# Performance work log

Measured on AMD Instinct MI355X. Metric: run time of the kernel, lower is better.

Reference implementation:

```python
import jax, jax.numpy as jnp
import numpy as np

HEADS = 8

def setup_inputs() -> dict:
    key = jax.random.key(0)
    ks = jax.random.split(key, 6)
    b, c, w, h = 4, 512, 48, 48
    qc, vc = 512, 512
    s = 1.0 / np.sqrt(c)  # orthogonal-init-like scale for 1x1 conv weights
    return {
        "x": jax.random.normal(ks[0], (b, c, w, h), dtype=jnp.float32),
        "Wq": jax.random.normal(ks[1], (qc, c), dtype=jnp.float32) * s,
        "Wk": jax.random.normal(ks[2], (qc, c), dtype=jnp.float32) * s,
        "Wv": jax.random.normal(ks[3], (vc, c), dtype=jnp.float32) * s,
        "Wsc": jax.random.normal(ks[4], (vc, c), dtype=jnp.float32) * s,
        "gamma": jax.random.normal(ks[5], (1, vc, 1, 1), dtype=jnp.float32),
    }


def reference(x, Wq, Wk, Wv, Wsc, gamma):
    b, c, w, h = x.shape
    n = w * h
    dq = Wq.shape[0] // HEADS
    dv = Wv.shape[0] // HEADS
    # 1x1 convs are channel matmuls
    q = jnp.einsum('bchw,oc->bohw', x, Wq).reshape(b, HEADS, dq, n)
    k = jnp.einsum('bchw,oc->bohw', x, Wk).reshape(b, HEADS, dq, n)
    v = jnp.einsum('bchw,oc->bohw', x, Wv).reshape(b, HEADS, dv, n)
    # attention scores over spatial tokens (no scaling in original)
    attn = jax.nn.softmax(jnp.einsum('bhdn,bhdm->bhnm', q, k), axis=-1)
    out = jnp.einsum('bhnm,bhdm->bnhd', attn, v)  # (b, n, heads, dv)
    out = out.reshape(b, w, h, HEADS * dv).transpose(0, 3, 1, 2)  # head-major channels
    sc = jnp.einsum('bchw,oc->bohw', x, Wsc)
    return gamma * out + sc
```

## Files before the change

kernel.cpp:

```cpp
#include <hip/hip_runtime.h>

#define HEADS 8
static constexpr int BSZ = 4;
static constexpr int CCH = 512;
static constexpr int NSP = 2304;
static constexpr int DH  = 64;

typedef _Float16 f16x8 __attribute__((ext_vector_type(8)));
typedef _Float16 f16x2 __attribute__((ext_vector_type(2)));
typedef float f32x4 __attribute__((ext_vector_type(4)));
typedef float f32x16 __attribute__((ext_vector_type(16)));
typedef int i32x4 __attribute__((ext_vector_type(4)));
typedef unsigned short u16;
typedef unsigned int u32;

__device__ __forceinline__ u16 f2h(float f) {
  _Float16 h = (_Float16)f;
  return __builtin_bit_cast(u16, h);
}

__device__ __forceinline__ void gl_lds16(const void* g, void* l) {
  __builtin_amdgcn_global_load_lds(
      (const __attribute__((address_space(1))) u32*)g,
      (__attribute__((address_space(3))) u32*)l, 16, 0, 0);
}

__global__ void k_cvt_w(const float* __restrict__ w0, const float* __restrict__ w1,
                        const float* __restrict__ w2, const float* __restrict__ w3,
                        u16* __restrict__ dst) {
  int wsel = blockIdx.y;
  const float* src = wsel == 0 ? w0 : wsel == 1 ? w1 : wsel == 2 ? w2 : w3;
  int i = (blockIdx.x * 256 + threadIdx.x) * 4;
  float4 v = *(const float4*)(src + i);
  ushort4 o;
  o.x = f2h(v.x); o.y = f2h(v.y); o.z = f2h(v.z); o.w = f2h(v.w);
  *(ushort4*)(dst + (size_t)wsel * CCH * CCH + i) = o;
}

__global__ void k_cvt_x(const float* __restrict__ x, u16* __restrict__ xT) {
  __shared__ u16 t[64][66];
  int b = blockIdx.z, c0 = blockIdx.y * 64, n0 = blockIdx.x * 64;
  int col = threadIdx.x & 63, rb = threadIdx.x >> 6;
#pragma unroll
  for (int rr = 0; rr < 16; rr++) {
    int r = rr * 4 + rb;
    t[r][col] = f2h(x[((size_t)b * CCH + c0 + r) * NSP + n0 + col]);
  }
  __syncthreads();
#pragma unroll
  for (int rr = 0; rr < 16; rr++) {
    int r = rr * 4 + rb;
    xT[((size_t)b * NSP + n0 + r) * CCH + c0 + col] = t[col][r];
  }
}

__global__ __launch_bounds__(256) void k_proj(const u16* __restrict__ Wall,
    const u16* __restrict__ xT, u16* __restrict__ Qo, u16* __restrict__ Ko,
    u16* __restrict__ Vo, float* __restrict__ SCo) {
  __shared__ u16 smem[17408];
  u16* At = smem;
  u16* Bt = smem + 8192;
  int z = blockIdx.z, b = z >> 2, wsel = z & 3;
  int o0 = blockIdx.y * 128, n0 = blockIdx.x * 128;
  int tid = threadIdx.x, lane = tid & 63, wv = tid >> 6;
  int wr = wv >> 1, wc = wv & 1;
  const u16* Asrc = Wall + (size_t)wsel * CCH * CCH + (size_t)o0 * CCH;
  const u16* Bsrc = xT + ((size_t)b * NSP + n0) * CCH;
  f32x4 acc[4][4] = {};
  for (int kc = 0; kc < CCH; kc += 64) {
    __syncthreads();
#pragma unroll
    for (int i = 0; i < 4; i++) {
      int ch = (wv * 4 + i) * 64 + lane;
      int row = ch >> 3, cc = ch & 7;
      gl_lds16(Asrc + (size_t)row * CCH + kc + ((cc ^ (row & 7)) << 3), At + (wv * 4 + i) * 512);
      gl_lds16(Bsrc + (size_t)row * CCH + kc + ((cc ^ (row & 7)) << 3), Bt + (wv * 4 + i) * 512);
    }
    __syncthreads();
#pragma unroll
    for (int ks = 0; ks < 2; ks++) {
      f16x8 af[4], bfr[4];
#pragma unroll
      for (int f = 0; f < 4; f++) {
        int orow = wr * 64 + f * 16 + (lane & 15);
        int nrow = wc * 64 + f * 16 + (lane & 15);
        int k8 = (lane >> 4) + ks * 4;
        af[f]  = *(const f16x8*)(At + orow * 64 + ((k8 ^ (orow & 7)) << 3));
        bfr[f] = *(const f16x8*)(Bt + nrow * 64 + ((k8 ^ (nrow & 7)) << 3));
      }
#pragma unroll
      for (int i = 0; i < 4; i++)
#pragma unroll
        for (int j = 0; j < 4; j++)
          acc[i][j] = __builtin_amdgcn_mfma_f32_16x16x32_f16(af[i], bfr[j], acc[i][j], 0, 0, 0);
    }
  }
  if (wsel >= 2) {
#pragma unroll
    for (int i = 0; i < 4; i++)
#pragma unroll
      for (int j = 0; j < 4; j++)
#pragma unroll
        for (int r = 0; r < 4; r++) {
          int o = o0 + wr * 64 + i * 16 + ((lane >> 4) << 2) + r;
          int n = n0 + wc * 64 + j * 16 + (lane & 15);
          size_t idx = ((size_t)b * CCH + o) * NSP + n;
          if (wsel == 3) SCo[idx] = acc[i][j][r];
          else           Vo[idx]  = f2h(acc[i][j][r]);
        }
  } else {
    __syncthreads();
    u16* stash = smem;
#pragma unroll
    for (int i = 0; i < 4; i++)
#pragma unroll
      for (int j = 0; j < 4; j++)
#pragma unroll
        for (int r = 0; r < 4; r++) {
          int ol = wr * 64 + i * 16 + ((lane >> 4) << 2) + r;
          int nl = wc * 64 + j * 16 + (lane & 15);
          stash[nl * 136 + ol] = f2h(acc[i][j][r]);
        }
    __syncthreads();
    u16* dst = wsel ? Ko : Qo;
    int hl = tid >> 7, nn = tid & 127;
    int h = (o0 >> 6) + hl;
    size_t base = ((size_t)(b * HEADS + h) * NSP + n0 + nn) * DH;
#pragma unroll
    for (int c2 = 0; c2 < 8; c2++)
      *(int4*)(dst + base + c2 * 8) = *(const int4*)(stash + nn * 136 + hl * 64 + c2 * 8);
  }
}

__device__ __forceinline__ void stage_kv(const u16* Ksrc, const u16* Vsrc,
                                         u16* Kb, u16* Vb, int bsel, int m0, int tid) {
#pragma unroll
  for (int i = 0; i < 4; i++) {
    int ch = i * 128 + tid;
    int row = ch >> 3, cc = ch & 7;
    gl_lds16(Ksrc + (size_t)(m0 + row) * DH + ((cc ^ (row & 7)) << 3),
             Kb + bsel * 4096 + ch * 8);
    gl_lds16(Vsrc + (size_t)row * NSP + m0 + ((cc ^ (row & 7)) << 3),
             Vb + bsel * 4096 + ch * 8);
  }
}

__global__ __launch_bounds__(128) void k_attn(const u16* __restrict__ Qw,
    const u16* __restrict__ Kw, const u16* __restrict__ Vw,
    const float* __restrict__ gamma, float* __restrict__ out) {
  __shared__ u16 smem[16384];
  u16* Kb = smem;
  u16* Vb = smem + 8192;
  int qt = blockIdx.x, bh = blockIdx.y;
  int b = bh >> 3, h = bh & 7;
  int tid = threadIdx.x, lane = tid & 63, wv = tid >> 6;
  int l31 = lane & 31, hi = lane >> 5;
  int q0w = qt * 64 + wv * 32;
  const u16* Ksrc = Kw + (size_t)bh * NSP * DH;
  const u16* Vsrc = Vw + ((size_t)b * CCH + h * DH) * NSP;

  f16x8 qf[4];
  const u16* Qbase = Qw + ((size_t)bh * NSP + q0w + l31) * DH + hi * 8;
#pragma unroll
  for (int kd = 0; kd < 4; kd++)
    qf[kd] = *(const f16x8*)(Qbase + kd * 16);

  float mrun = -1e30f, lrun = 0.f;
  f32x16 acc0 = {}, acc1 = {};

  stage_kv(Ksrc, Vsrc, Kb, Vb, 0, 0, tid);
  __syncthreads();

  for (int mt = 0; mt < NSP / 64; mt++) {
    int cur = mt & 1;
    if (mt + 1 < NSP / 64) stage_kv(Ksrc, Vsrc, Kb, Vb, cur ^ 1, (mt + 1) * 64, tid);

    f32x16 s0 = {}, s1 = {};
#pragma unroll
    for (int kd = 0; kd < 4; kd++) {
      int cc = 2 * kd + hi;
      int r0 = l31, r1 = 32 + l31;
      f16x8 k0 = *(const f16x8*)(Kb + cur * 4096 + r0 * 64 + ((cc ^ (r0 & 7)) << 3));
      f16x8 k1 = *(const f16x8*)(Kb + cur * 4096 + r1 * 64 + ((cc ^ (r1 & 7)) << 3));
      s0 = __builtin_amdgcn_mfma_f32_32x32x16_f16(k0, qf[kd], s0, 0, 0, 0);
      s1 = __builtin_amdgcn_mfma_f32_32x32x16_f16(k1, qf[kd], s1, 0, 0, 0);
    }

    float tm = fmaxf(s0[0], s1[0]);
#pragma unroll
    for (int r = 1; r < 16; r++) tm = fmaxf(tm, fmaxf(s0[r], s1[r]));
    tm = fmaxf(tm, __shfl_xor(tm, 32));
    if (__any(tm > mrun + 8.0f)) {
      float mnew = fmaxf(mrun, tm);
      float scl = __expf(mrun - mnew);
      mrun = mnew;
      lrun *= scl;
#pragma unroll
      for (int r = 0; r < 16; r++) {
        float sq = __shfl(scl, (r & 3) + 8 * (r >> 2) + 4 * hi);
        acc0[r] *= sq;
        acc1[r] *= sq;
      }
    }
    float ts = 0.f;
    u32 P2[2][4][2];
#pragma unroll
    for (int s2 = 0; s2 < 4; s2++)
#pragma unroll
      for (int c = 0; c < 2; c++) {
        float a0 = __expf(s0[4 * s2 + 2 * c] - mrun);
        float b0 = __expf(s0[4 * s2 + 2 * c + 1] - mrun);
        float a1 = __expf(s1[4 * s2 + 2 * c] - mrun);
        float b1 = __expf(s1[4 * s2 + 2 * c + 1] - mrun);
        ts += (a0 + b0) + (a1 + b1);
        P2[0][s2][c] = __builtin_bit_cast(u32, __builtin_amdgcn_cvt_pkrtz(a0, b0));
        P2[1][s2][c] = __builtin_bit_cast(u32, __builtin_amdgcn_cvt_pkrtz(a1, b1));
      }
    ts += __shfl_xor(ts, 32);
    lrun += ts;

#pragma unroll
    for (int s = 0; s < 4; s++) {
      int blk = s >> 1, par = s & 1;
      int T[4];
#pragma unroll
      for (int c = 0; c < 2; c++) {
        int x = (int)P2[blk][2 * par][c];
        int y = (int)P2[blk][2 * par + 1][c];
        int xs = __shfl_xor(x, 32);
        int ys = __shfl_xor(y, 32);
        T[c]     = hi ? ys : x;
        T[c + 2] = hi ? y  : xs;
      }
      f16x8 pa = __builtin_bit_cast(f16x8, (i32x4){T[0], T[1], T[2], T[3]});
      int ccv = 2 * s + hi;
      {
        int row = l31;
        f16x8 vb = *(const f16x8*)(Vb + cur * 4096 + row * 64 + ((ccv ^ (row & 7)) << 3));
        acc0 = __builtin_amdgcn_mfma_f32_32x32x16_f16(pa, vb, acc0, 0, 0, 0);
      }
      {
        int row = 32 + l31;
        f16x8 vb = *(const f16x8*)(Vb + cur * 4096 + row * 64 + ((ccv ^ (row & 7)) << 3));
        acc1 = __builtin_amdgcn_mfma_f32_32x32x16_f16(pa, vb, acc1, 0, 0, 0);
      }
    }
    __syncthreads();
  }

  float inv = 1.0f / lrun;
  float invq[16];
#pragma unroll
  for (int r = 0; r < 16; r++)
    invq[r] = __shfl(inv, (r & 3) + 8 * (r >> 2) + 4 * hi);
  size_t outbase = ((size_t)b * CCH + h * DH) * NSP;
#pragma unroll
  for (int dblk = 0; dblk < 2; dblk++) {
    int d = dblk * 32 + l31;
    float g = gamma[h * DH + d];
    float* orow = out + outbase + (size_t)d * NSP + q0w;
#pragma unroll
    for (int s2 = 0; s2 < 4; s2++) {
      int n = 8 * s2 + 4 * hi;
      f32x4 o;
#pragma unroll
      for (int t = 0; t < 4; t++) {
        int r = 4 * s2 + t;
        float a = dblk ? acc1[r] : acc0[r];
        o[t] = a * invq[r] * g;
      }
      f32x4 sc = *(const f32x4*)(orow + n);
      *(f32x4*)(orow + n) = o + sc;
    }
  }
}

extern "C" void kernel_launch(void* const* d_in, const int* in_sizes, int n_in,
                              void* d_out, int out_size, void* d_ws, size_t ws_size,
                              hipStream_t stream) {
  const float* x     = (const float*)d_in[0];
  const float* Wq    = (const float*)d_in[1];
  const float* Wk    = (const float*)d_in[2];
  const float* Wv    = (const float*)d_in[3];
  const float* Wsc   = (const float*)d_in[4];
  const float* gamma = (const float*)d_in[5];
  float* out = (float*)d_out;

  u16* xT   = (u16*)d_ws;
  u16* Wall = xT + (size_t)BSZ * NSP * CCH;
  u16* Qw   = Wall + (size_t)4 * CCH * CCH;
  u16* Kw   = Qw + (size_t)BSZ * CCH * NSP;
  u16* Vw   = Kw + (size_t)BSZ * CCH * NSP;

  hipLaunchKernelGGL(k_cvt_w, dim3(CCH * CCH / 1024, 4), dim3(256), 0, stream,
                     Wq, Wk, Wv, Wsc, Wall);
  hipLaunchKernelGGL(k_cvt_x, dim3(NSP / 64, CCH / 64, BSZ), dim3(256), 0, stream, x, xT);
  hipLaunchKernelGGL(k_proj, dim3(NSP / 128, CCH / 128, BSZ * 4), dim3(256), 0, stream,
                     Wall, xT, Qw, Kw, Vw, out);
  hipLaunchKernelGGL(k_attn, dim3(NSP / 64, BSZ * HEADS), dim3(128), 0, stream,
                     Qw, Kw, Vw, gamma, out);
}
```

Measured before the change: 172.4 us.

## Split attention KV range across two wave groups and fold log2e into Q

```diff
diff --git a/kernel.cpp b/kernel.cpp
--- a/kernel.cpp
+++ b/kernel.cpp
@@ -7,7 +7,6 @@
 static constexpr int DH  = 64;
 
 typedef _Float16 f16x8 __attribute__((ext_vector_type(8)));
-typedef _Float16 f16x2 __attribute__((ext_vector_type(2)));
 typedef float f32x4 __attribute__((ext_vector_type(4)));
 typedef float f32x16 __attribute__((ext_vector_type(16)));
 typedef int i32x4 __attribute__((ext_vector_type(4)));
@@ -111,6 +110,7 @@
   } else {
     __syncthreads();
     u16* stash = smem;
+    float qs = (wsel == 0) ? 1.4426950408889634f : 1.0f;
 #pragma unroll
     for (int i = 0; i < 4; i++)
 #pragma unroll
@@ -119,7 +119,7 @@
         for (int r = 0; r < 4; r++) {
           int ol = wr * 64 + i * 16 + ((lane >> 4) << 2) + r;
           int nl = wc * 64 + j * 16 + (lane & 15);
-          stash[nl * 136 + ol] = f2h(acc[i][j][r]);
+          stash[nl * 136 + ol] = f2h(acc[i][j][r] * qs);
         }
     __syncthreads();
     u16* dst = wsel ? Ko : Qo;
@@ -132,32 +132,32 @@
   }
 }
 
-__device__ __forceinline__ void stage_kv(const u16* Ksrc, const u16* Vsrc,
-                                         u16* Kb, u16* Vb, int bsel, int m0, int tid) {
-#pragma unroll
-  for (int i = 0; i < 4; i++) {
-    int ch = i * 128 + tid;
+__device__ __forceinline__ void stage_kv256(const u16* Ksrc, const u16* Vsrc,
+                                            u16* Kb, u16* Vb, int m0, int gid) {
+#pragma unroll
+  for (int i = 0; i < 2; i++) {
+    int ch = i * 256 + gid;
     int row = ch >> 3, cc = ch & 7;
-    gl_lds16(Ksrc + (size_t)(m0 + row) * DH + ((cc ^ (row & 7)) << 3),
-             Kb + bsel * 4096 + ch * 8);
-    gl_lds16(Vsrc + (size_t)row * NSP + m0 + ((cc ^ (row & 7)) << 3),
-             Vb + bsel * 4096 + ch * 8);
-  }
-}
-
-__global__ __launch_bounds__(128) void k_attn(const u16* __restrict__ Qw,
+    gl_lds16(Ksrc + (size_t)(m0 + row) * DH + ((cc ^ (row & 7)) << 3), Kb + ch * 8);
+    gl_lds16(Vsrc + (size_t)row * NSP + m0 + ((cc ^ (row & 7)) << 3), Vb + ch * 8);
+  }
+}
+
+__global__ __launch_bounds__(512, 4) void k_attn(const u16* __restrict__ Qw,
     const u16* __restrict__ Kw, const u16* __restrict__ Vw,
     const float* __restrict__ gamma, float* __restrict__ out) {
-  __shared__ u16 smem[16384];
-  u16* Kb = smem;
-  u16* Vb = smem + 8192;
+  __shared__ u16 smem[32768];
   int qt = blockIdx.x, bh = blockIdx.y;
   int b = bh >> 3, h = bh & 7;
   int tid = threadIdx.x, lane = tid & 63, wv = tid >> 6;
   int l31 = lane & 31, hi = lane >> 5;
-  int q0w = qt * 64 + wv * 32;
+  int qh = wv & 3, tp = wv >> 2;
+  int gid = tid & 255;
+  int q0w = qt * 128 + qh * 32;
   const u16* Ksrc = Kw + (size_t)bh * NSP * DH;
   const u16* Vsrc = Vw + ((size_t)b * CCH + h * DH) * NSP;
+  u16* Kb = smem + tp * 16384;
+  u16* Vb = Kb + 8192;
 
   f16x8 qf[4];
   const u16* Qbase = Qw + ((size_t)bh * NSP + q0w + l31) * DH + hi * 8;
@@ -168,31 +168,39 @@
   float mrun = -1e30f, lrun = 0.f;
   f32x16 acc0 = {}, acc1 = {};
 
-  stage_kv(Ksrc, Vsrc, Kb, Vb, 0, 0, tid);
+  stage_kv256(Ksrc, Vsrc, Kb, Vb, tp * 64, gid);
   __syncthreads();
 
-  for (int mt = 0; mt < NSP / 64; mt++) {
-    int cur = mt & 1;
-    if (mt + 1 < NSP / 64) stage_kv(Ksrc, Vsrc, Kb, Vb, cur ^ 1, (mt + 1) * 64, tid);
+  const int NT = NSP / 128;
+  for (int it = 0; it < NT; it++) {
+    int cur = it & 1;
+    if (it + 1 < NT)
+      stage_kv256(Ksrc, Vsrc, Kb + (cur ^ 1) * 4096, Vb + (cur ^ 1) * 4096,
+                  (tp + 2 * (it + 1)) * 64, gid);
+    const u16* Kc = Kb + cur * 4096;
+    const u16* Vc = Vb + cur * 4096;
 
     f32x16 s0 = {}, s1 = {};
 #pragma unroll
     for (int kd = 0; kd < 4; kd++) {
       int cc = 2 * kd + hi;
       int r0 = l31, r1 = 32 + l31;
-      f16x8 k0 = *(const f16x8*)(Kb + cur * 4096 + r0 * 64 + ((cc ^ (r0 & 7)) << 3));
-      f16x8 k1 = *(const f16x8*)(Kb + cur * 4096 + r1 * 64 + ((cc ^ (r1 & 7)) << 3));
+      f16x8 k0 = *(const f16x8*)(Kc + r0 * 64 + ((cc ^ (r0 & 7)) << 3));
+      f16x8 k1 = *(const f16x8*)(Kc + r1 * 64 + ((cc ^ (r1 & 7)) << 3));
       s0 = __builtin_amdgcn_mfma_f32_32x32x16_f16(k0, qf[kd], s0, 0, 0, 0);
       s1 = __builtin_amdgcn_mfma_f32_32x32x16_f16(k1, qf[kd], s1, 0, 0, 0);
     }
 
-    float tm = fmaxf(s0[0], s1[0]);
-#pragma unroll
-    for (int r = 1; r < 16; r++) tm = fmaxf(tm, fmaxf(s0[r], s1[r]));
+    float a8[8];
+#pragma unroll
+    for (int i = 0; i < 8; i++)
+      a8[i] = fmaxf(fmaxf(s0[2 * i], s0[2 * i + 1]), fmaxf(s1[2 * i], s1[2 * i + 1]));
+    float tm = fmaxf(fmaxf(fmaxf(a8[0], a8[1]), fmaxf(a8[2], a8[3])),
+                     fmaxf(fmaxf(a8[4], a8[5]), fmaxf(a8[6], a8[7])));
     tm = fmaxf(tm, __shfl_xor(tm, 32));
-    if (__any(tm > mrun + 8.0f)) {
+    if (__any(tm > mrun + 11.5f)) {
       float mnew = fmaxf(mrun, tm);
-      float scl = __expf(mrun - mnew);
+      float scl = exp2f(mrun - mnew);
       mrun = mnew;
       lrun *= scl;
 #pragma unroll
@@ -202,20 +210,21 @@
         acc1[r] *= sq;
       }
     }
-    float ts = 0.f;
+    float tsp[4] = {0.f, 0.f, 0.f, 0.f};
     u32 P2[2][4][2];
 #pragma unroll
     for (int s2 = 0; s2 < 4; s2++)
 #pragma unroll
       for (int c = 0; c < 2; c++) {
-        float a0 = __expf(s0[4 * s2 + 2 * c] - mrun);
-        float b0 = __expf(s0[4 * s2 + 2 * c + 1] - mrun);
-        float a1 = __expf(s1[4 * s2 + 2 * c] - mrun);
-        float b1 = __expf(s1[4 * s2 + 2 * c + 1] - mrun);
-        ts += (a0 + b0) + (a1 + b1);
+        float a0 = exp2f(s0[4 * s2 + 2 * c] - mrun);
+        float b0 = exp2f(s0[4 * s2 + 2 * c + 1] - mrun);
+        float a1 = exp2f(s1[4 * s2 + 2 * c] - mrun);
+        float b1 = exp2f(s1[4 * s2 + 2 * c + 1] - mrun);
+        tsp[s2] += (a0 + b0) + (a1 + b1);
         P2[0][s2][c] = __builtin_bit_cast(u32, __builtin_amdgcn_cvt_pkrtz(a0, b0));
         P2[1][s2][c] = __builtin_bit_cast(u32, __builtin_amdgcn_cvt_pkrtz(a1, b1));
       }
+    float ts = (tsp[0] + tsp[1]) + (tsp[2] + tsp[3]);
     ts += __shfl_xor(ts, 32);
     lrun += ts;
 
@@ -236,41 +245,65 @@
       int ccv = 2 * s + hi;
       {
         int row = l31;
-        f16x8 vb = *(const f16x8*)(Vb + cur * 4096 + row * 64 + ((ccv ^ (row & 7)) << 3));
+        f16x8 vb = *(const f16x8*)(Vc + row * 64 + ((ccv ^ (row & 7)) << 3));
         acc0 = __builtin_amdgcn_mfma_f32_32x32x16_f16(pa, vb, acc0, 0, 0, 0);
       }
       {
         int row = 32 + l31;
-        f16x8 vb = *(const f16x8*)(Vb + cur * 4096 + row * 64 + ((ccv ^ (row & 7)) << 3));
+        f16x8 vb = *(const f16x8*)(Vc + row * 64 + ((ccv ^ (row & 7)) << 3));
         acc1 = __builtin_amdgcn_mfma_f32_32x32x16_f16(pa, vb, acc1, 0, 0, 0);
       }
     }
     __syncthreads();
   }
 
-  float inv = 1.0f / lrun;
-  float invq[16];
-#pragma unroll
-  for (int r = 0; r < 16; r++)
-    invq[r] = __shfl(inv, (r & 3) + 8 * (r >> 2) + 4 * hi);
-  size_t outbase = ((size_t)b * CCH + h * DH) * NSP;
-#pragma unroll
-  for (int dblk = 0; dblk < 2; dblk++) {
-    int d = dblk * 32 + l31;
-    float g = gamma[h * DH + d];
-    float* orow = out + outbase + (size_t)d * NSP + q0w;
-#pragma unroll
-    for (int s2 = 0; s2 < 4; s2++) {
-      int n = 8 * s2 + 4 * hi;
-      f32x4 o;
-#pragma unroll
-      for (int t = 0; t < 4; t++) {
-        int r = 4 * s2 + t;
-        float a = dblk ? acc1[r] : acc0[r];
-        o[t] = a * invq[r] * g;
-      }
-      f32x4 sc = *(const f32x4*)(orow + n);
-      *(f32x4*)(orow + n) = o + sc;
+  float* sf = (float*)smem;
+  if (tp) {
+#pragma unroll
+    for (int r = 0; r < 16; r++) {
+      sf[qh * 2048 + r * 64 + lane] = acc0[r];
+      sf[qh * 2048 + (16 + r) * 64 + lane] = acc1[r];
+    }
+    if (lane < 32) {
+      sf[8192 + qh * 64 + l31] = mrun;
+      sf[8192 + qh * 64 + 32 + l31] = lrun;
+    }
+  }
+  __syncthreads();
+  if (!tp) {
+    float mb = sf[8192 + qh * 64 + l31];
+    float lb = sf[8192 + qh * 64 + 32 + l31];
+    float M = fmaxf(mrun, mb);
+    float fa = exp2f(mrun - M), fb = exp2f(mb - M);
+    float linv = 1.0f / (lrun * fa + lb * fb);
+    fa *= linv; fb *= linv;
+    float faq[16], fbq[16];
+#pragma unroll
+    for (int r = 0; r < 16; r++) {
+      int qloc = (r & 3) + 8 * (r >> 2) + 4 * hi;
+      faq[r] = __shfl(fa, qloc);
+      fbq[r] = __shfl(fb, qloc);
+    }
+    size_t outbase = ((size_t)b * CCH + h * DH) * NSP;
+#pragma unroll
+    for (int dblk = 0; dblk < 2; dblk++) {
+      int d = dblk * 32 + l31;
+      float g = gamma[h * DH + d];
+      float* orow = out + outbase + (size_t)d * NSP + q0w;
+#pragma unroll
+      for (int s2 = 0; s2 < 4; s2++) {
+        int n = 8 * s2 + 4 * hi;
+        f32x4 o;
+#pragma unroll
+        for (int t = 0; t < 4; t++) {
+          int r = 4 * s2 + t;
+          float oa = dblk ? acc1[r] : acc0[r];
+          float ob = sf[qh * 2048 + (dblk * 16 + r) * 64 + lane];
+          o[t] = (oa * faq[r] + ob * fbq[r]) * g;
+        }
+        f32x4 sc = *(const f32x4*)(orow + n);
+        *(f32x4*)(orow + n) = o + sc;
+      }
     }
   }
 }
@@ -297,6 +330,6 @@
   hipLaunchKernelGGL(k_cvt_x, dim3(NSP / 64, CCH / 64, BSZ), dim3(256), 0, stream, x, xT);
   hipLaunchKernelGGL(k_proj, dim3(NSP / 128, CCH / 128, BSZ * 4), dim3(256), 0, stream,
                      Wall, xT, Qw, Kw, Vw, out);
-  hipLaunchKernelGGL(k_attn, dim3(NSP / 64, BSZ * HEADS), dim3(128), 0, stream,
+  hipLaunchKernelGGL(k_attn, dim3(NSP / 128, BSZ * HEADS), dim3(512), 0, stream,
                      Qw, Kw, Vw, gamma, out);
 }
```

New measurement: 176.3 us. +2.3%, slower.

## Restructure attention loop with 32-key tiles, exp2 softmax, permlane swap, priorities

Applied to the files above, without the earlier changes.

```diff
diff --git a/kernel.cpp b/kernel.cpp
--- a/kernel.cpp
+++ b/kernel.cpp
@@ -7,7 +7,6 @@
 static constexpr int DH  = 64;
 
 typedef _Float16 f16x8 __attribute__((ext_vector_type(8)));
-typedef _Float16 f16x2 __attribute__((ext_vector_type(2)));
 typedef float f32x4 __attribute__((ext_vector_type(4)));
 typedef float f32x16 __attribute__((ext_vector_type(16)));
 typedef int i32x4 __attribute__((ext_vector_type(4)));
@@ -17,6 +16,10 @@
 __device__ __forceinline__ u16 f2h(float f) {
   _Float16 h = (_Float16)f;
   return __builtin_bit_cast(u16, h);
+}
+
+__device__ __forceinline__ float fexp2(float x) {
+  return __builtin_amdgcn_exp2f(x);
 }
 
 __device__ __forceinline__ void gl_lds16(const void* g, void* l) {
@@ -111,6 +114,7 @@
   } else {
     __syncthreads();
     u16* stash = smem;
+    float qs = (wsel == 0) ? 1.4426950408889634f : 1.0f;
 #pragma unroll
     for (int i = 0; i < 4; i++)
 #pragma unroll
@@ -119,7 +123,7 @@
         for (int r = 0; r < 4; r++) {
           int ol = wr * 64 + i * 16 + ((lane >> 4) << 2) + r;
           int nl = wc * 64 + j * 16 + (lane & 15);
-          stash[nl * 136 + ol] = f2h(acc[i][j][r]);
+          stash[nl * 136 + ol] = f2h(acc[i][j][r] * qs);
         }
     __syncthreads();
     u16* dst = wsel ? Ko : Qo;
@@ -132,25 +136,10 @@
   }
 }
 
-__device__ __forceinline__ void stage_kv(const u16* Ksrc, const u16* Vsrc,
-                                         u16* Kb, u16* Vb, int bsel, int m0, int tid) {
-#pragma unroll
-  for (int i = 0; i < 4; i++) {
-    int ch = i * 128 + tid;
-    int row = ch >> 3, cc = ch & 7;
-    gl_lds16(Ksrc + (size_t)(m0 + row) * DH + ((cc ^ (row & 7)) << 3),
-             Kb + bsel * 4096 + ch * 8);
-    gl_lds16(Vsrc + (size_t)row * NSP + m0 + ((cc ^ (row & 7)) << 3),
-             Vb + bsel * 4096 + ch * 8);
-  }
-}
-
 __global__ __launch_bounds__(128) void k_attn(const u16* __restrict__ Qw,
     const u16* __restrict__ Kw, const u16* __restrict__ Vw,
     const float* __restrict__ gamma, float* __restrict__ out) {
-  __shared__ u16 smem[16384];
-  u16* Kb = smem;
-  u16* Vb = smem + 8192;
+  __shared__ u16 smem[8192];
   int qt = blockIdx.x, bh = blockIdx.y;
   int b = bh >> 3, h = bh & 7;
   int tid = threadIdx.x, lane = tid & 63, wv = tid >> 6;
@@ -158,6 +147,35 @@
   int q0w = qt * 64 + wv * 32;
   const u16* Ksrc = Kw + (size_t)bh * NSP * DH;
   const u16* Vsrc = Vw + ((size_t)b * CCH + h * DH) * NSP;
+  u16* Kb0 = smem;
+  u16* Kb1 = smem + 4096;
+
+  int ch0 = tid, ch1 = 128 + tid;
+  int mk0 = ch0 >> 3, pk0 = ch0 & 7, mk1 = ch1 >> 3, pk1 = ch1 & 7;
+  const u16* kc0 = Ksrc + mk0 * DH + ((pk0 ^ (mk0 & 7)) << 3);
+  const u16* kc1 = Ksrc + mk1 * DH + ((pk1 ^ (mk1 & 7)) << 3);
+  int dv0 = ch0 >> 2, pv0 = ch0 & 3, dv1 = ch1 >> 2, pv1 = ch1 & 3;
+  const u16* vc0 = Vsrc + dv0 * NSP + ((pv0 ^ ((dv0 >> 1) & 3)) << 3);
+  const u16* vc1 = Vsrc + dv1 * NSP + ((pv1 ^ ((dv1 >> 1) & 3)) << 3);
+
+#define STAGE(KB)                                  \
+  do {                                             \
+    gl_lds16(kc0, (KB) + ch0 * 8);                 \
+    gl_lds16(kc1, (KB) + ch1 * 8);                 \
+    gl_lds16(vc0, (KB) + 2048 + ch0 * 8);          \
+    gl_lds16(vc1, (KB) + 2048 + ch1 * 8);          \
+    kc0 += 32 * DH; kc1 += 32 * DH;                \
+    vc0 += 32; vc1 += 32;                          \
+  } while (0)
+
+  int kswz = l31 & 7, vswz = (l31 >> 1) & 3;
+  int kro = l31 * 64;
+  int ko[4], vo[2];
+#pragma unroll
+  for (int kd = 0; kd < 4; kd++) ko[kd] = ((2 * kd + hi) ^ kswz) << 3;
+#pragma unroll
+  for (int s = 0; s < 2; s++) vo[s] = ((2 * s + hi) ^ vswz) << 3;
+  int vr0 = l31 * 32, vr1 = (32 + l31) * 32;
 
   f16x8 qf[4];
   const u16* Qbase = Qw + ((size_t)bh * NSP + q0w + l31) * DH + hi * 8;
@@ -168,83 +186,79 @@
   float mrun = -1e30f, lrun = 0.f;
   f32x16 acc0 = {}, acc1 = {};
 
-  stage_kv(Ksrc, Vsrc, Kb, Vb, 0, 0, tid);
+#define COMPUTE(KB)                                                          \
+  do {                                                                       \
+    const u16* Kc = (KB);                                                    \
+    const u16* Vc = (KB) + 2048;                                             \
+    f32x16 s0 = {};                                                          \
+    __builtin_amdgcn_s_setprio(1);                                           \
+    _Pragma("unroll")                                                        \
+    for (int kd = 0; kd < 4; kd++) {                                         \
+      f16x8 k0 = *(const f16x8*)(Kc + kro + ko[kd]);                         \
+      s0 = __builtin_amdgcn_mfma_f32_32x32x16_f16(k0, qf[kd], s0, 0, 0, 0);  \
+    }                                                                        \
+    __builtin_amdgcn_s_setprio(0);                                           \
+    float m0a = fmaxf(fmaxf(s0[0], s0[1]), s0[2]);                           \
+    float m0b = fmaxf(fmaxf(s0[3], s0[4]), s0[5]);                           \
+    float m0c = fmaxf(fmaxf(s0[6], s0[7]), s0[8]);                           \
+    float m0d = fmaxf(fmaxf(s0[9], s0[10]), s0[11]);                         \
+    float m0e = fmaxf(fmaxf(s0[12], s0[13]), s0[14]);                        \
+    float tm = fmaxf(fmaxf(fmaxf(m0a, m0b), fmaxf(m0c, m0d)),                \
+                     fmaxf(m0e, s0[15]));                                    \
+    tm = fmaxf(tm, __shfl_xor(tm, 32));                                      \
+    if (__any(tm > mrun + 11.5f)) {                                          \
+      float mnew = fmaxf(mrun, tm);                                          \
+      float scl = fexp2(mrun - mnew);                                        \
+      mrun = mnew;                                                           \
+      lrun *= scl;                                                           \
+      _Pragma("unroll")                                                      \
+      for (int r = 0; r < 16; r++) {                                         \
+        float sq = __shfl(scl, (r & 3) + 8 * (r >> 2) + 4 * hi);             \
+        acc0[r] *= sq;                                                       \
+        acc1[r] *= sq;                                                       \
+      }                                                                      \
+    }                                                                        \
+    float ts = 0.f;                                                          \
+    u32 P2[4][2];                                                            \
+    _Pragma("unroll")                                                        \
+    for (int s2 = 0; s2 < 4; s2++)                                           \
+      _Pragma("unroll")                                                      \
+      for (int c = 0; c < 2; c++) {                                          \
+        float a = fexp2(s0[4 * s2 + 2 * c] - mrun);                          \
+        float bb = fexp2(s0[4 * s2 + 2 * c + 1] - mrun);                     \
+        ts += a + bb;                                                        \
+        P2[s2][c] = __builtin_bit_cast(u32, __builtin_amdgcn_cvt_pkrtz(a, bb)); \
+      }                                                                      \
+    ts += __shfl_xor(ts, 32);                                                \
+    lrun += ts;                                                              \
+    _Pragma("unroll")                                                        \
+    for (int s = 0; s < 2; s++) {                                            \
+      int x0 = (int)P2[2 * s][0], y0 = (int)P2[2 * s + 1][0];                \
+      int x1 = (int)P2[2 * s][1], y1 = (int)P2[2 * s + 1][1];                \
+      asm("v_permlane32_swap_b32 %0, %1" : "+v"(x0), "+v"(y0));              \
+      asm("v_permlane32_swap_b32 %0, %1" : "+v"(x1), "+v"(y1));              \
+      f16x8 pa = __builtin_bit_cast(f16x8, (i32x4){x0, x1, y0, y1});         \
+      __builtin_amdgcn_s_setprio(1);                                         \
+      {                                                                      \
+        f16x8 vb = *(const f16x8*)(Vc + vr0 + vo[s]);                        \
+        acc0 = __builtin_amdgcn_mfma_f32_32x32x16_f16(pa, vb, acc0, 0, 0, 0);\
+      }                                                                      \
+      {                                                                      \
+        f16x8 vb = *(const f16x8*)(Vc + vr1 + vo[s]);                        \
+        acc1 = __builtin_amdgcn_mfma_f32_32x32x16_f16(pa, vb, acc1, 0, 0, 0);\
+      }                                                                      \
+      __builtin_amdgcn_s_setprio(0);                                         \
+    }                                                                        \
+  } while (0)
+
+  STAGE(Kb0);
   __syncthreads();
-
-  for (int mt = 0; mt < NSP / 64; mt++) {
-    int cur = mt & 1;
-    if (mt + 1 < NSP / 64) stage_kv(Ksrc, Vsrc, Kb, Vb, cur ^ 1, (mt + 1) * 64, tid);
-
-    f32x16 s0 = {}, s1 = {};
-#pragma unroll
-    for (int kd = 0; kd < 4; kd++) {
-      int cc = 2 * kd + hi;
-      int r0 = l31, r1 = 32 + l31;
-      f16x8 k0 = *(const f16x8*)(Kb + cur * 4096 + r0 * 64 + ((cc ^ (r0 & 7)) << 3));
-      f16x8 k1 = *(const f16x8*)(Kb + cur * 4096 + r1 * 64 + ((cc ^ (r1 & 7)) << 3));
-      s0 = __builtin_amdgcn_mfma_f32_32x32x16_f16(k0, qf[kd], s0, 0, 0, 0);
-      s1 = __builtin_amdgcn_mfma_f32_32x32x16_f16(k1, qf[kd], s1, 0, 0, 0);
-    }
-
-    float tm = fmaxf(s0[0], s1[0]);
-#pragma unroll
-    for (int r = 1; r < 16; r++) tm = fmaxf(tm, fmaxf(s0[r], s1[r]));
-    tm = fmaxf(tm, __shfl_xor(tm, 32));
-    if (__any(tm > mrun + 8.0f)) {
-      float mnew = fmaxf(mrun, tm);
-      float scl = __expf(mrun - mnew);
-      mrun = mnew;
-      lrun *= scl;
-#pragma unroll
-      for (int r = 0; r < 16; r++) {
-        float sq = __shfl(scl, (r & 3) + 8 * (r >> 2) + 4 * hi);
-        acc0[r] *= sq;
-        acc1[r] *= sq;
-      }
-    }
-    float ts = 0.f;
-    u32 P2[2][4][2];
-#pragma unroll
-    for (int s2 = 0; s2 < 4; s2++)
-#pragma unroll
-      for (int c = 0; c < 2; c++) {
-        float a0 = __expf(s0[4 * s2 + 2 * c] - mrun);
-        float b0 = __expf(s0[4 * s2 + 2 * c + 1] - mrun);
-        float a1 = __expf(s1[4 * s2 + 2 * c] - mrun);
-        float b1 = __expf(s1[4 * s2 + 2 * c + 1] - mrun);
-        ts += (a0 + b0) + (a1 + b1);
-        P2[0][s2][c] = __builtin_bit_cast(u32, __builtin_amdgcn_cvt_pkrtz(a0, b0));
-        P2[1][s2][c] = __builtin_bit_cast(u32, __builtin_amdgcn_cvt_pkrtz(a1, b1));
-      }
-    ts += __shfl_xor(ts, 32);
-    lrun += ts;
-
-#pragma unroll
-    for (int s = 0; s < 4; s++) {
-      int blk = s >> 1, par = s & 1;
-      int T[4];
-#pragma unroll
-      for (int c = 0; c < 2; c++) {
-        int x = (int)P2[blk][2 * par][c];
-        int y = (int)P2[blk][2 * par + 1][c];
-        int xs = __shfl_xor(x, 32);
-        int ys = __shfl_xor(y, 32);
-        T[c]     = hi ? ys : x;
-        T[c + 2] = hi ? y  : xs;
-      }
-      f16x8 pa = __builtin_bit_cast(f16x8, (i32x4){T[0], T[1], T[2], T[3]});
-      int ccv = 2 * s + hi;
-      {
-        int row = l31;
-        f16x8 vb = *(const f16x8*)(Vb + cur * 4096 + row * 64 + ((ccv ^ (row & 7)) << 3));
-        acc0 = __builtin_amdgcn_mfma_f32_32x32x16_f16(pa, vb, acc0, 0, 0, 0);
-      }
-      {
-        int row = 32 + l31;
-        f16x8 vb = *(const f16x8*)(Vb + cur * 4096 + row * 64 + ((ccv ^ (row & 7)) << 3));
-        acc1 = __builtin_amdgcn_mfma_f32_32x32x16_f16(pa, vb, acc1, 0, 0, 0);
-      }
-    }
+  for (int it2 = 0; it2 < 36; it2++) {
+    STAGE(Kb1);
+    COMPUTE(Kb0);
+    __syncthreads();
+    if (it2 < 35) STAGE(Kb0);
+    COMPUTE(Kb1);
     __syncthreads();
   }
 
@@ -273,6 +287,8 @@
       *(f32x4*)(orow + n) = o + sc;
     }
   }
+#undef STAGE
+#undef COMPUTE
 }
 
 extern "C" void kernel_launch(void* const* d_in, const int* in_sizes, int n_in,
```

Result: faster. 167.5 us (-2.8%).
